# Kernel tuning notes

Measured on AMD Instinct MI355X. Metric: run time of the kernel, lower is better.

The kernel has to match this reference:

```python
import jax, jax.numpy as jnp
import numpy as np

EMBED = 1024
N_HEAD = 16
D_HID = EMBED // N_HEAD
R_FF = 4
D_FF = EMBED * R_FF
LN_EPS = 1e-5


def layer_norm(x, gamma, beta):
    mu = jnp.mean(x, axis=-1, keepdims=True)
    var = jnp.var(x, axis=-1, keepdims=True)
    return (x - mu) * jax.lax.rsqrt(var + LN_EPS) * gamma + beta


def setup_inputs() -> dict:
    key = jax.random.key(0)
    ks = jax.random.split(key, 10)
    B, S = 4, 2048
    # torch nn.Linear stores weight as [out, in]; y = x @ W.T
    def xavier(k, shape):
        fan_out, fan_in = shape
        lim = np.sqrt(6.0 / (fan_in + fan_out))
        return jax.random.uniform(k, shape, jnp.float32, -lim, lim)
    return {
        "x": jax.random.normal(ks[0], (B, S, EMBED), jnp.float32),
        "Wq": xavier(ks[1], (EMBED, EMBED)),
        "Wk": xavier(ks[2], (EMBED, EMBED)),
        "Wv": xavier(ks[3], (EMBED, EMBED)),
        "Wo": xavier(ks[4], (EMBED, EMBED)),
        "bo": jnp.zeros((EMBED,), jnp.float32),
        "ln1_g": jnp.ones((EMBED,), jnp.float32),
        "ln1_b": jnp.zeros((EMBED,), jnp.float32),
        "ln2_g": jnp.ones((EMBED,), jnp.float32),
        "ln2_b": jnp.zeros((EMBED,), jnp.float32),
        "W1": jax.random.normal(ks[5], (D_FF, EMBED), jnp.float32) * np.sqrt(2.0 / EMBED),
        "b1": jnp.zeros((D_FF,), jnp.float32),
        "W2": xavier(ks[6], (EMBED, D_FF)),
        "b2": jnp.zeros((EMBED,), jnp.float32),
    }


def reference(x, Wq, Wk, Wv, Wo, bo, ln1_g, ln1_b, ln2_g, ln2_b, W1, b1, W2, b2):
    B, S, E = x.shape
    scaling = 1.0 / np.sqrt(D_HID)
    # --- attention (pre-LN), dropout = identity (eval) ---
    xn = layer_norm(x, ln1_g, ln1_b)
    q = (xn @ Wq.T).reshape(B, S, N_HEAD, D_HID) * scaling
    k = (xn @ Wk.T).reshape(B, S, N_HEAD, D_HID)
    v = (xn @ Wv.T).reshape(B, S, N_HEAD, D_HID)
    scores = jnp.einsum("bqhd,bkhd->bhqk", q, k)
    attn = jax.nn.softmax(scores, axis=-1)
    out = jnp.einsum("bhqk,bkhd->bqhd", attn, v).reshape(B, S, E)
    out = out @ Wo.T + bo
    x = x + out
    # --- feed-forward (pre-LN) ---
    xn = layer_norm(x, ln2_g, ln2_b)
    h = jax.nn.relu(xn @ W1.T + b1)
    x = x + (h @ W2.T + b2)
    return x
```

## Files before the change

kernel.cpp:

```cpp
#include <hip/hip_runtime.h>
#include <hip/hip_bf16.h>
#include <cstdint>


typedef __attribute__((ext_vector_type(8))) short bf16x8;
typedef __attribute__((ext_vector_type(4))) float f32x4;

#define LDSAS __attribute__((address_space(3)))
#define GLBAS __attribute__((address_space(1)))

#define CQK 0.18033688011112044f

__device__ __forceinline__ unsigned short f2bf(float f) {
  union { float f; unsigned u; } c; c.f = f;
  unsigned u = c.u + 0x7fffu + ((c.u >> 16) & 1u);
  return (unsigned short)(u >> 16);
}

__device__ __forceinline__ unsigned pk2(float a, float b) {
  __hip_bfloat162 h = __float22bfloat162_rn(make_float2(a, b));
  union { __hip_bfloat162 h; unsigned u; } c; c.h = h; return c.u;
}

__device__ __forceinline__ void async16(const unsigned short* g, unsigned short* l) {
  __builtin_amdgcn_global_load_lds((const GLBAS unsigned int*)g,
                                   (LDSAS unsigned int*)l, 16, 0, 0);
}

__global__ void cvt_all(const float* __restrict__ q, const float* __restrict__ k,
                        const float* __restrict__ v, const float* __restrict__ o,
                        const float* __restrict__ w1, const float* __restrict__ w2,
                        unsigned short* __restrict__ wsb) {
  const long i = (long)blockIdx.x * 256 + threadIdx.x;
  const float* src; unsigned short* dst; long off;
  if (i < 1048576) {
    const long seg = i >> 18, o4 = i & 262143;
    src = (seg == 0) ? q : (seg == 1) ? k : (seg == 2) ? v : o;
    dst = wsb + ((seg == 3) ? 3145728L : seg * 1048576L);
    off = o4;
  } else if (i < 2097152) {
    src = w1; dst = wsb + 4194304; off = i - 1048576;
  } else {
    src = w2; dst = wsb + 8388608; off = i - 2097152;
  }
  const float4 vv = ((const float4*)src)[off];
  ushort4 r;
  r.x = f2bf(vv.x); r.y = f2bf(vv.y); r.z = f2bf(vv.z); r.w = f2bf(vv.w);
  ((ushort4*)dst)[off] = r;
}

__global__ void ln_fwd(const float* __restrict__ x, const float* __restrict__ g,
                       const float* __restrict__ bb, unsigned short* __restrict__ outp) {
  const int row = blockIdx.x, tid = threadIdx.x;
  const float4 v = ((const float4*)(x + (long)row * 1024))[tid];
  float s  = v.x + v.y + v.z + v.w;
  float sq = v.x * v.x + v.y * v.y + v.z * v.z + v.w * v.w;
#pragma unroll
  for (int off = 1; off < 64; off <<= 1) {
    s  += __shfl_xor(s, off);
    sq += __shfl_xor(sq, off);
  }
  __shared__ float red[8];
  const int wv = tid >> 6, lane = tid & 63;
  if (lane == 0) { red[wv] = s; red[4 + wv] = sq; }
  __syncthreads();
  s  = red[0] + red[1] + red[2] + red[3];
  sq = red[4] + red[5] + red[6] + red[7];
  const float mu  = s * (1.f / 1024.f);
  const float var = sq * (1.f / 1024.f) - mu * mu;
  const float rstd = rsqrtf(var + 1e-5f);
  const float4 gv = ((const float4*)g)[tid];
  const float4 bv = ((const float4*)bb)[tid];
  ushort4 o;
  o.x = f2bf((v.x - mu) * rstd * gv.x + bv.x);
  o.y = f2bf((v.y - mu) * rstd * gv.y + bv.y);
  o.z = f2bf((v.z - mu) * rstd * gv.z + bv.z);
  o.w = f2bf((v.w - mu) * rstd * gv.w + bv.w);
  ((ushort4*)(outp + (long)row * 1024))[tid] = o;
}

template <int EPI>
__launch_bounds__(256, 3)
__global__ void gemm_bt(const unsigned short* __restrict__ A,
                        const unsigned short* __restrict__ B,
                        void* __restrict__ Cout,
                        const float* __restrict__ bias,
                        const float* __restrict__ res,
                        int M, int N, int K) {
  __shared__ __align__(16) unsigned short As[128 * 64];
  __shared__ __align__(16) unsigned short Bs[128 * 64];
  const int tid  = threadIdx.x;
  const int lane = tid & 63;
  const int wvu  = __builtin_amdgcn_readfirstlane(tid >> 6);
  const int quad = lane >> 4, l16 = lane & 15;
  const int wm = wvu >> 1, wn = wvu & 1;

  const int gx = gridDim.x;
  const int id = blockIdx.y * gx + blockIdx.x;
  const int xcd = id & 7, slot = id >> 3;
  const int by = xcd * 8 + (slot & 7);
  const int bx = slot >> 3;
  const long m0 = (long)by * 128, n0 = (long)bx * 128;

  f32x4 acc[4][4];
#pragma unroll
  for (int i = 0; i < 4; i++)
#pragma unroll
    for (int j = 0; j < 4; j++) acc[i][j] = (f32x4){0.f, 0.f, 0.f, 0.f};

  const int rxA = l16 & 7;
  const int c0A = quad ^ rxA;
  int srow[4], sgc[4];
#pragma unroll
  for (int j = 0; j < 4; ++j) {
    const int s = wvu * 256 + j * 64 + lane;
    srow[j] = s >> 3;
    sgc[j] = ((s & 7) ^ (srow[j] & 7)) * 8;
  }

  for (int k0 = 0; k0 < K; k0 += 64) {
    __syncthreads();
#pragma unroll
    for (int j = 0; j < 4; ++j) {
      const int db = (wvu * 256 + j * 64) * 8;
      async16(A + (m0 + srow[j]) * K + k0 + sgc[j], As + db);
      async16(B + (n0 + srow[j]) * K + k0 + sgc[j], Bs + db);
    }
    __syncthreads();

#pragma unroll
    for (int kc = 0; kc < 2; ++kc) {
      const int ch = (c0A ^ (kc * 4)) * 8;
      bf16x8 af[4], bfr[4];
#pragma unroll
      for (int t = 0; t < 4; ++t) {
        af[t]  = *(const bf16x8*)(As + (wm * 64 + t * 16 + l16) * 64 + ch);
        bfr[t] = *(const bf16x8*)(Bs + (wn * 64 + t * 16 + l16) * 64 + ch);
      }
#pragma unroll
      for (int mt = 0; mt < 4; ++mt)
#pragma unroll
        for (int nt = 0; nt < 4; ++nt)
          acc[mt][nt] = __builtin_amdgcn_mfma_f32_16x16x32_bf16(af[mt], bfr[nt],
                                                                acc[mt][nt], 0, 0, 0);
    }
  }

#pragma unroll
  for (int nt = 0; nt < 4; ++nt) {
    const long col = n0 + wn * 64 + nt * 16 + l16;
    float bv = 0.f;
    if (EPI == 1 || EPI == 2) bv = bias[col];
    const float scl = (EPI == 3 && col < 1024) ? CQK : 1.0f;
#pragma unroll
    for (int mt = 0; mt < 4; ++mt) {
#pragma unroll
      for (int r = 0; r < 4; ++r) {
        const long row = m0 + wm * 64 + mt * 16 + quad * 4 + r;
        const long idx = row * (long)N + col;
        float v = acc[mt][nt][r];
        if (EPI == 0) {
          ((unsigned short*)Cout)[idx] = f2bf(v);
        } else if (EPI == 1) {
          ((float*)Cout)[idx] = v + bv + res[idx];
        } else if (EPI == 2) {
          v += bv;
          ((unsigned short*)Cout)[idx] = f2bf(v > 0.f ? v : 0.f);
        } else {
          ((unsigned short*)Cout)[idx] = f2bf(v * scl);
        }
      }
    }
  }
}

__global__ void vprep(const unsigned short* __restrict__ qkv,
                      unsigned short* __restrict__ vt) {
  __shared__ unsigned short T[64 * 68];
  const int tid = threadIdx.x;
  const int t = blockIdx.x;
  const int bh = blockIdx.y;
  const int b = bh >> 4, h = bh & 15;
  const long base = ((long)b * 2048 + t * 64) * 3072 + 2048 + h * 64;
#pragma unroll
  for (int i = 0; i < 4; ++i) {
    int c = i * 256 + tid;
    int r = c >> 4, d4 = (c & 15) * 4;
    *(ushort4*)(T + r * 68 + d4) = *(const ushort4*)(qkv + base + (long)r * 3072 + d4);
  }
  __syncthreads();
  unsigned short* out = vt + ((long)bh * 32 + t) * 4096;
#pragma unroll
  for (int i = 0; i < 4; ++i) {
    int u = i * 256 + tid;
    int c = u >> 1, half = u & 1;
    int d = c >> 3;
    int k = ((c & 7) - d) & 7;
    int kvp4 = k * 8 + half * 4;
    int sk = (kvp4 & 32) | ((kvp4 & 4) << 2) | ((kvp4 & 16) >> 1) | ((kvp4 & 8) >> 1);
    ushort4 o;
    o.x = T[(sk + 0) * 68 + d];
    o.y = T[(sk + 1) * 68 + d];
    o.z = T[(sk + 2) * 68 + d];
    o.w = T[(sk + 3) * 68 + d];
    *(ushort4*)(out + u * 4) = o;
  }
}

__launch_bounds__(256, 4)
__global__ void attn_fwd(const unsigned short* __restrict__ qkv,
                         const unsigned short* __restrict__ vt,
                         unsigned short* __restrict__ outp) {
  __shared__ __align__(16) unsigned short lds[16384];

  const int tid = threadIdx.x;
  const int lane = tid & 63;
  const int wv = __builtin_amdgcn_readfirstlane(tid >> 6);
  const int quad = lane >> 4, l16 = lane & 15;

  const int id = blockIdx.y * 16 + blockIdx.x;
  const int xcd = id & 7, slot = id >> 3;
  const int bh = xcd * 8 + (slot >> 4);
  const int qt = slot & 15;
  const int b = bh >> 4, h = bh & 15;
  const long rowbase = (long)b * 2048;
  const int hoff = h * 64;

  const int rot0 = (quad + l16) & 7;
  const int rot1 = rot0 ^ 4;

  bf16x8 bq[2][2];
#pragma unroll
  for (int s = 0; s < 2; ++s) {
    const long qrow = rowbase + qt * 128 + wv * 32 + s * 16 + l16;
    const unsigned short* qp = qkv + qrow * 3072 + hoff;
    bq[s][0] = *(const bf16x8*)(qp + quad * 8);
    bq[s][1] = *(const bf16x8*)(qp + (quad ^ 4) * 8);
  }
  __builtin_amdgcn_sched_barrier(0);

  const int c0 = wv * 64 + lane;
  const int r0 = c0 >> 3;
  const int ks = ((c0 & 7) - r0) & 7;
  const unsigned short* kptr = qkv + (rowbase + r0) * 3072 + 1024 + hoff + ks * 8;
  const unsigned short* vptr = vt + (long)bh * 131072 + (long)c0 * 8;

  auto stage = [&](int t) {
    unsigned short* kdst = lds + (t & 1) * 4096 + wv * 512;
    unsigned short* vdst = lds + 8192 + (t & 1) * 4096 + wv * 512;
    const unsigned short* kp = kptr + (long)t * 64 * 3072;
    const unsigned short* vp = vptr + (long)t * 4096;
#pragma unroll
    for (int j = 0; j < 2; ++j) {
      async16(kp + (long)j * 32 * 3072, kdst + j * 2048);
      async16(vp + j * 2048, vdst + j * 2048);
    }
  };

  bf16x8 ones;
#pragma unroll
  for (int i = 0; i < 8; ++i) ones[i] = (short)0x3F80;

  f32x4 oacc[2][4], lacc[2];
#pragma unroll
  for (int s = 0; s < 2; ++s) {
    lacc[s] = (f32x4){0.f, 0.f, 0.f, 0.f};
#pragma unroll
    for (int i = 0; i < 4; ++i) oacc[s][i] = (f32x4){0.f, 0.f, 0.f, 0.f};
  }

  stage(0); stage(1);
  asm volatile("s_waitcnt vmcnt(4)" ::: "memory");
  __builtin_amdgcn_s_barrier();
  __builtin_amdgcn_sched_barrier(0);

  for (int kt = 0; kt < 32; ++kt) {
    const unsigned short* Kb = lds + (kt & 1) * 4096;
    const unsigned short* Vb = lds + 8192 + (kt & 1) * 4096;

    f32x4 sacc[2][4];
    __builtin_amdgcn_s_setprio(1);
#pragma unroll
    for (int t = 0; t < 4; ++t) {
      const int ar = t * 16 + l16;
      bf16x8 ak0 = *(const bf16x8*)(Kb + ar * 64 + rot0 * 8);
      bf16x8 ak1 = *(const bf16x8*)(Kb + ar * 64 + rot1 * 8);
#pragma unroll
      for (int s = 0; s < 2; ++s) {
        f32x4 z = (f32x4){0.f, 0.f, 0.f, 0.f};
        z = __builtin_amdgcn_mfma_f32_16x16x32_bf16(ak0, bq[s][0], z, 0, 0, 0);
        sacc[s][t] = __builtin_amdgcn_mfma_f32_16x16x32_bf16(ak1, bq[s][1], z, 0, 0, 0);
      }
    }
    __builtin_amdgcn_s_setprio(0);

    union APU { unsigned u[4]; bf16x8 v; } ap[2][2];
#pragma unroll
    for (int s = 0; s < 2; ++s)
#pragma unroll
      for (int hf = 0; hf < 2; ++hf) {
#pragma unroll
        for (int t = 0; t < 2; ++t) {
          const f32x4 sv = sacc[s][hf * 2 + t];
          const float p0 = __builtin_amdgcn_exp2f(sv[0]);
          const float p1 = __builtin_amdgcn_exp2f(sv[1]);
          const float p2 = __builtin_amdgcn_exp2f(sv[2]);
          const float p3 = __builtin_amdgcn_exp2f(sv[3]);
          ap[s][hf].u[t * 2 + 0] = pk2(p0, p1);
          ap[s][hf].u[t * 2 + 1] = pk2(p2, p3);
        }
        lacc[s] = __builtin_amdgcn_mfma_f32_16x16x32_bf16(ap[s][hf].v, ones,
                                                          lacc[s], 0, 0, 0);
      }

    __builtin_amdgcn_s_setprio(1);
#pragma unroll
    for (int hf = 0; hf < 2; ++hf) {
      const int vbase = (hf ? rot1 : rot0) * 8;
#pragma unroll
      for (int dt = 0; dt < 4; ++dt) {
        bf16x8 bv = *(const bf16x8*)(Vb + vbase + (dt * 16 + l16) * 64);
#pragma unroll
        for (int s = 0; s < 2; ++s)
          oacc[s][dt] = __builtin_amdgcn_mfma_f32_16x16x32_bf16(ap[s][hf].v, bv,
                                                                oacc[s][dt], 0, 0, 0);
      }
    }
    __builtin_amdgcn_s_setprio(0);

    if (kt == 31) break;
    __builtin_amdgcn_s_barrier();
    __builtin_amdgcn_sched_barrier(0);
    if (kt + 2 < 32) {
      stage(kt + 2);
      asm volatile("s_waitcnt vmcnt(4)" ::: "memory");
    } else {
      asm volatile("s_waitcnt vmcnt(0)" ::: "memory");
    }
    __builtin_amdgcn_s_barrier();
    __builtin_amdgcn_sched_barrier(0);
  }

#pragma unroll
  for (int s = 0; s < 2; ++s) {
    float linv[4];
#pragma unroll
    for (int r = 0; r < 4; ++r) linv[r] = 1.f / lacc[s][r];
#pragma unroll
    for (int dt = 0; dt < 4; ++dt)
#pragma unroll
      for (int r = 0; r < 4; ++r) {
        const long row = rowbase + qt * 128 + wv * 32 + s * 16 + quad * 4 + r;
        outp[row * 1024 + hoff + dt * 16 + l16] = f2bf(oacc[s][dt][r] * linv[r]);
      }
  }
}

extern "C" void kernel_launch(void* const* d_in, const int* in_sizes, int n_in,
                              void* d_out, int out_size, void* d_ws, size_t ws_size,
                              hipStream_t stream) {
  (void)in_sizes; (void)n_in; (void)out_size; (void)ws_size;
  const float* x   = (const float*)d_in[0];
  const float* Wq  = (const float*)d_in[1];
  const float* Wk  = (const float*)d_in[2];
  const float* Wv  = (const float*)d_in[3];
  const float* Wo  = (const float*)d_in[4];
  const float* bo  = (const float*)d_in[5];
  const float* g1  = (const float*)d_in[6];
  const float* be1 = (const float*)d_in[7];
  const float* g2  = (const float*)d_in[8];
  const float* be2 = (const float*)d_in[9];
  const float* W1  = (const float*)d_in[10];
  const float* bf1 = (const float*)d_in[11];
  const float* W2  = (const float*)d_in[12];
  const float* bf2 = (const float*)d_in[13];

  char* ws = (char*)d_ws;
  unsigned short* wqkv  = (unsigned short*)(ws);
  unsigned short* wo    = (unsigned short*)(ws + 6291456);
  unsigned short* w1    = (unsigned short*)(ws + 8388608);
  unsigned short* w2    = (unsigned short*)(ws + 16777216);
  unsigned short* xn    = (unsigned short*)(ws + 25165824);
  unsigned short* big   = (unsigned short*)(ws + 41943040);
  unsigned short* attnb = (unsigned short*)(ws + 109051904);
  float*          x1    = (float*)(ws + 125829120);
  unsigned short* vtg   = xn;

  cvt_all<<<12288, 256, 0, stream>>>(Wq, Wk, Wv, Wo, W1, W2, wqkv);

  ln_fwd<<<8192, 256, 0, stream>>>(x, g1, be1, xn);
  gemm_bt<3><<<dim3(24, 64), 256, 0, stream>>>(xn, wqkv, big, nullptr, nullptr,
                                               8192, 3072, 1024);
  vprep<<<dim3(32, 64), 256, 0, stream>>>(big, vtg);
  attn_fwd<<<dim3(16, 64), 256, 0, stream>>>(big, vtg, attnb);
  gemm_bt<1><<<dim3(8, 64), 256, 0, stream>>>(attnb, wo, x1, bo, x,
                                              8192, 1024, 1024);
  ln_fwd<<<8192, 256, 0, stream>>>(x1, g2, be2, xn);
  gemm_bt<2><<<dim3(32, 64), 256, 0, stream>>>(xn, w1, big, bf1, nullptr,
                                               8192, 4096, 1024);
  gemm_bt<1><<<dim3(8, 64), 256, 0, stream>>>(big, w2, (float*)d_out, bf2, x1,
                                              8192, 1024, 4096);
}
```

Before: 485.3 us.

## Add specialized 8-wave pipelined GEMM for FFN down-projection

Replaces the generic gemm_bt call for the W2 down-projection (K=4096) with a dedicated 512-thread kernel that uses 128x256 tiles, double-buffered LDS staging in halves, and interleaved async loads with MFMA phases under barriers and s_setprio. It also remaps block IDs so that blocks sharing M rows land on the same XCD for L2 reuse. The aim is to hide global-load latency and raise MFMA utilisation on the largest-K GEMM. In exchange it needs 96KB of dynamic LDS, a one-time attribute call, and a hand-tuned schedule with fragile waitcnt accounting.

```diff
diff --git a/kernel.cpp b/kernel.cpp
--- a/kernel.cpp
+++ b/kernel.cpp
@@ -169,6 +169,192 @@
         } else {
           ((unsigned short*)Cout)[idx] = f2bf(v * scl);
         }
+      }
+    }
+  }
+}
+
+#define W2_LDA(AF, BUF, H)                                                      \
+  do {                                                                          \
+    const unsigned short* _p = As + ((BUF) * 2 + (H)) * 4096;                   \
+    _Pragma("unroll") for (int _m = 0; _m < 2; ++_m) {                          \
+      AF[_m][0] = *(const bf16x8*)(_p + (_m * 32 + rA) * 64 + chk0);            \
+      AF[_m][1] = *(const bf16x8*)(_p + (_m * 32 + rA) * 64 + chk1);            \
+    }                                                                           \
+  } while (0)
+
+#define W2_LDB(BF, BUF, H)                                                      \
+  do {                                                                          \
+    const unsigned short* _p = Bs + ((BUF) * 2 + (H)) * 8192;                   \
+    _Pragma("unroll") for (int _n = 0; _n < 2; ++_n) {                          \
+      BF[_n][0] = *(const bf16x8*)(_p + (_n * 64 + rB) * 64 + chk0);            \
+      BF[_n][1] = *(const bf16x8*)(_p + (_n * 64 + rB) * 64 + chk1);            \
+    }                                                                           \
+  } while (0)
+
+#define W2_MFMA(AH, BH, AF, BF)                                                 \
+  do {                                                                          \
+    _Pragma("unroll") for (int _m = 0; _m < 2; ++_m)                            \
+    _Pragma("unroll") for (int _n = 0; _n < 2; ++_n) {                          \
+      acc[(AH) * 2 + _m][(BH) * 2 + _n] =                                       \
+          __builtin_amdgcn_mfma_f32_16x16x32_bf16(                              \
+              AF[_m][0], BF[_n][0], acc[(AH) * 2 + _m][(BH) * 2 + _n], 0, 0, 0);\
+      acc[(AH) * 2 + _m][(BH) * 2 + _n] =                                       \
+          __builtin_amdgcn_mfma_f32_16x16x32_bf16(                              \
+              AF[_m][1], BF[_n][1], acc[(AH) * 2 + _m][(BH) * 2 + _n], 0, 0, 0);\
+    }                                                                           \
+  } while (0)
+
+#define PH_MID()                                                                \
+  __builtin_amdgcn_s_barrier();                                                 \
+  asm volatile("s_waitcnt lgkmcnt(0)" ::: "memory");                            \
+  __builtin_amdgcn_sched_barrier(0);                                            \
+  __builtin_amdgcn_s_setprio(1)
+
+#define PH_END()                                                                \
+  __builtin_amdgcn_s_setprio(0);                                                \
+  __builtin_amdgcn_sched_barrier(0);                                            \
+  __builtin_amdgcn_s_barrier();                                                 \
+  __builtin_amdgcn_sched_barrier(0)
+
+__launch_bounds__(512, 2)
+__global__ void gemm_w2(const unsigned short* __restrict__ A,
+                        const unsigned short* __restrict__ B,
+                        float* __restrict__ Cout,
+                        const float* __restrict__ bias,
+                        const float* __restrict__ res,
+                        int M, int N, int K) {
+  extern __shared__ __align__(16) unsigned short lds[];
+  unsigned short* As = lds;
+  unsigned short* Bs = lds + 16384;
+
+  const int tid  = threadIdx.x;
+  const int lane = tid & 63;
+  const int wv   = __builtin_amdgcn_readfirstlane(tid >> 6);
+  const int quad = lane >> 4, l16 = lane & 15;
+  const int wm = wv >> 2, wn = wv & 3;
+
+  const int id = blockIdx.x;
+  const int xcd = id & 7, slot = id >> 3;
+  const int by = xcd * 8 + (slot & 7);
+  const int bx = slot >> 3;
+  const long m0 = (long)by * 128, n0 = (long)bx * 256;
+
+  const int s0 = wv * 64 + lane;
+  const int r0 = s0 >> 3;
+  const int c0 = (s0 ^ r0) & 7;
+  const int s1 = 512 + s0;
+  const int r1 = s1 >> 3;
+  const int c1 = (s1 ^ r1) & 7;
+  const long rt0 = (long)r0 * K + c0 * 8;
+  const long rt1 = (long)r1 * K + c1 * 8;
+  const unsigned short* Ab = A + m0 * K;
+  const unsigned short* Bb = B + n0 * K;
+
+  const int rA = wm * 16 + l16;
+  const int rB = wn * 16 + l16;
+  const int chk0 = (quad ^ (l16 & 7)) * 8;
+  const int chk1 = chk0 ^ 32;
+
+  f32x4 acc[4][4];
+#pragma unroll
+  for (int a_ = 0; a_ < 4; ++a_)
+#pragma unroll
+    for (int b_ = 0; b_ < 4; ++b_) acc[a_][b_] = (f32x4){0.f, 0.f, 0.f, 0.f};
+
+  auto stgA = [&](int b, int h, long kk) {
+    const unsigned short* s = Ab + (long)h * 64 * K + kk;
+    async16(s + rt0, As + (b * 2 + h) * 4096 + wv * 512);
+  };
+  auto stgB = [&](int b, int h, long kk) {
+    const unsigned short* s = Bb + (long)h * 128 * K + kk;
+    unsigned short* d = Bs + (b * 2 + h) * 8192 + wv * 512;
+    async16(s + rt0, d);
+    async16(s + rt1, d + 4096);
+  };
+
+  stgA(0, 0, 0); stgB(0, 1, 0); stgA(0, 1, 0); stgB(0, 0, 0);
+  stgA(1, 0, 64); stgB(1, 1, 64); stgA(1, 1, 64);
+  asm volatile("s_waitcnt vmcnt(4)" ::: "memory");
+  __builtin_amdgcn_s_barrier();
+  __builtin_amdgcn_sched_barrier(0);
+
+  const int NI = K >> 7;
+  for (int it = 0; it < NI; ++it) {
+    const long kt  = (long)it * 128;
+    const long ku  = kt + 64;
+    const long kt2 = kt + 128;
+    const long kt3 = kt + 192;
+    const bool more = (it + 1 < NI);
+
+    {
+      bf16x8 a0[2][2], a1[2][2], b0[2][2], b1[2][2];
+      W2_LDA(a0, 0, 0); W2_LDB(b0, 0, 0);
+      stgB(1, 0, ku);
+      PH_MID();
+      W2_MFMA(0, 0, a0, b0);
+      PH_END();
+      W2_LDB(b1, 0, 1);
+      if (more) stgA(0, 0, kt2);
+      PH_MID();
+      W2_MFMA(0, 1, a0, b1);
+      PH_END();
+      W2_LDA(a1, 0, 1);
+      if (more) stgB(0, 1, kt2);
+      PH_MID();
+      W2_MFMA(1, 1, a1, b1);
+      PH_END();
+      W2_LDB(b0, 0, 0);
+      if (more) stgA(0, 1, kt2);
+      PH_MID();
+      W2_MFMA(1, 0, a1, b0);
+      __builtin_amdgcn_s_setprio(0);
+      __builtin_amdgcn_sched_barrier(0);
+      if (more) { asm volatile("s_waitcnt vmcnt(4)" ::: "memory"); }
+      else      { asm volatile("s_waitcnt vmcnt(0)" ::: "memory"); }
+      __builtin_amdgcn_s_barrier();
+      __builtin_amdgcn_sched_barrier(0);
+    }
+    {
+      bf16x8 a0[2][2], a1[2][2], b0[2][2], b1[2][2];
+      W2_LDA(a0, 1, 0); W2_LDB(b0, 1, 0);
+      if (more) stgB(0, 0, kt2);
+      PH_MID();
+      W2_MFMA(0, 0, a0, b0);
+      PH_END();
+      W2_LDB(b1, 1, 1);
+      if (more) stgA(1, 0, kt3);
+      PH_MID();
+      W2_MFMA(0, 1, a0, b1);
+      PH_END();
+      W2_LDA(a1, 1, 1);
+      if (more) stgB(1, 1, kt3);
+      PH_MID();
+      W2_MFMA(1, 1, a1, b1);
+      PH_END();
+      W2_LDB(b0, 1, 0);
+      if (more) stgA(1, 1, kt3);
+      PH_MID();
+      W2_MFMA(1, 0, a1, b0);
+      __builtin_amdgcn_s_setprio(0);
+      __builtin_amdgcn_sched_barrier(0);
+      if (more) { asm volatile("s_waitcnt vmcnt(4)" ::: "memory"); }
+      __builtin_amdgcn_s_barrier();
+      __builtin_amdgcn_sched_barrier(0);
+    }
+  }
+
+#pragma unroll
+  for (int nt = 0; nt < 4; ++nt) {
+    const long col = n0 + nt * 64 + wn * 16 + l16;
+    const float bv = bias[col];
+#pragma unroll
+    for (int mt = 0; mt < 4; ++mt) {
+#pragma unroll
+      for (int r = 0; r < 4; ++r) {
+        const long row = m0 + mt * 32 + wm * 16 + quad * 4 + r;
+        const long idx = row * (long)N + col;
+        Cout[idx] = acc[mt][nt][r] + bv + res[idx];
       }
     }
   }
@@ -375,6 +561,13 @@
   const float* W2  = (const float*)d_in[12];
   const float* bf2 = (const float*)d_in[13];
 
+  static bool s_attr = false;
+  if (!s_attr) {
+    hipFuncSetAttribute(reinterpret_cast<const void*>(&gemm_w2),
+                        hipFuncAttributeMaxDynamicSharedMemorySize, 98304);
+    s_attr = true;
+  }
+
   char* ws = (char*)d_ws;
   unsigned short* wqkv  = (unsigned short*)(ws);
   unsigned short* wo    = (unsigned short*)(ws + 6291456);
@@ -398,6 +591,6 @@
   ln_fwd<<<8192, 256, 0, stream>>>(x1, g2, be2, xn);
   gemm_bt<2><<<dim3(32, 64), 256, 0, stream>>>(xn, w1, big, bf1, nullptr,
                                                8192, 4096, 1024);
-  gemm_bt<1><<<dim3(8, 64), 256, 0, stream>>>(big, w2, (float*)d_out, bf2, x1,
-                                              8192, 1024, 4096);
-}
+  gemm_w2<<<dim3(256), 512, 98304, stream>>>(big, w2, (float*)d_out, bf2, x1,
+                                             8192, 1024, 4096);
+}
```

Result: faster. 474.8 us (-2.2%).
